# Optimization experiments

Hardware: AMD Instinct MI355X
Metric: run time of the kernel (lower is better)

Reference implementation:

```python
import jax, jax.numpy as jnp
import numpy as np

B, N, D_IN, D_OUT, H = 2, 2048, 1024, 1024, 16
HEAD_DIM = D_OUT // H


def setup_inputs() -> dict:
    key = jax.random.key(0)
    ks = jax.random.split(key, 8)
    s = 0.02
    return {
        "x": jax.random.normal(ks[0], (B, N, D_IN), dtype=jnp.float32),
        "Wq": jax.random.normal(ks[1], (D_IN, D_OUT), dtype=jnp.float32) * s,
        "Wk": jax.random.normal(ks[2], (D_IN, D_OUT), dtype=jnp.float32) * s,
        "Wv": jax.random.normal(ks[3], (D_IN, D_OUT), dtype=jnp.float32) * s,
        "Wo": jax.random.normal(ks[4], (D_OUT, D_OUT), dtype=jnp.float32) * s,
        "bo": jnp.zeros((D_OUT,), dtype=jnp.float32),
        "w": jax.random.uniform(ks[5], (H,), dtype=jnp.float32),
        "v": jax.random.uniform(ks[6], (H,), dtype=jnp.float32),
    }


def reference(x, Wq, Wk, Wv, Wo, bo, w, v):
    b, n, _ = x.shape
    h = w.shape[0]
    hd = Wq.shape[1] // h

    # QKV projections -> [b, h, n, hd]
    def proj(W):
        return (x @ W).reshape(b, n, h, hd).transpose(0, 2, 1, 3)

    q, k, val = proj(Wq), proj(Wk), proj(Wv)

    # relative-distance decay R_hat: [h, n, n]
    pos = jnp.arange(n)
    R = jnp.abs(pos[:, None] - pos[None, :]).astype(x.dtype)  # [n, n]
    wv = w[:, None, None]
    vv = v[:, None, None]
    R_hat = (1.0 + jnp.exp(vv)) / (1.0 + jnp.exp(vv - wv * R))  # [h, n, n]

    # ReLU(QK^T) * R_hat, causal mask, scaled softmax
    scores = jax.nn.relu(jnp.einsum("bhqd,bhkd->bhqk", q, k)) * R_hat[None]
    causal = jnp.triu(jnp.ones((n, n), dtype=bool), k=1)
    scores = jnp.where(causal[None, None], -jnp.inf, scores)
    attn = jax.nn.softmax(scores / np.sqrt(hd).astype(x.dtype), axis=-1)

    ctx = jnp.einsum("bhqk,bhkd->bhqd", attn, val)
    ctx = ctx.transpose(0, 2, 1, 3).reshape(b, n, h * hd)
    return ctx @ Wo + bo
```

## Files before the change

kernel.cpp:

```cpp
#include <hip/hip_runtime.h>

typedef unsigned short u16;
typedef unsigned int u32;
typedef __attribute__((ext_vector_type(8))) short bf16x8;
typedef __attribute__((ext_vector_type(4))) float f32x4;

__device__ __forceinline__ u16 f2bf(float f) {
    u32 u = __float_as_uint(f);
    u += 0x7fffu + ((u >> 16) & 1u);
    return (u16)(u >> 16);
}

#define GL2LDS(gp, lp)                                                                 \
    __builtin_amdgcn_global_load_lds((const __attribute__((address_space(1))) u32*)(const void*)(gp), \
                                     (__attribute__((address_space(3))) u32*)(void*)(lp), 16, 0, 0)

__global__ __launch_bounds__(256) void cast_kernel(const float* __restrict__ src,
                                                   u16* __restrict__ dst, int n4) {
    int i = blockIdx.x * 256 + threadIdx.x;
    if (i >= n4) return;
    float4 val = ((const float4*)src)[i];
    uint2 o;
    o.x = ((u32)f2bf(val.y) << 16) | f2bf(val.x);
    o.y = ((u32)f2bf(val.w) << 16) | f2bf(val.z);
    ((uint2*)dst)[i] = o;
}

__global__ __launch_bounds__(256) void transpose4(const float* __restrict__ Wq,
                                                  const float* __restrict__ Wk,
                                                  const float* __restrict__ Wv,
                                                  const float* __restrict__ Wo,
                                                  u16* __restrict__ Wcat,
                                                  u16* __restrict__ Wot) {
    __shared__ float tl[32][33];
    const int zi = blockIdx.z;
    const float* src = (zi == 0) ? Wq : (zi == 1) ? Wk : (zi == 2) ? Wv : Wo;
    u16* dst = (zi < 3) ? (Wcat + zi * 1048576) : Wot;
    const int tx = threadIdx.x & 31, ty = threadIdx.x >> 5;
    const int kt = blockIdx.y * 32, nt = blockIdx.x * 32;
#pragma unroll
    for (int j = 0; j < 4; ++j)
        tl[ty + j * 8][tx] = src[(kt + ty + j * 8) * 1024 + nt + tx];
    __syncthreads();
#pragma unroll
    for (int j = 0; j < 4; ++j)
        dst[(nt + ty + j * 8) * 1024 + kt + tx] = f2bf(tl[tx][ty + j * 8]);
}

__global__ __launch_bounds__(256) void rtab_kernel(const float* __restrict__ wp,
                                                   const float* __restrict__ vp,
                                                   float* __restrict__ tab,
                                                   u32* __restrict__ counter) {
    const int i = blockIdx.x * 256 + threadIdx.x;
    if (i == 0) counter[0] = 0u;
    const int h = i >> 11, d = i & 2047;
    const float vv = vp[h], ww = wp[h];
    tab[i] = (1.f + expf(vv)) / (1.f + expf(vv - ww * (float)d)) * 0.125f;
}

template <int MODE, int BN>
__global__ __launch_bounds__(256, 3) void gemm128(const u16* __restrict__ A,
                                                  const u16* __restrict__ Bt,
                                                  float* __restrict__ C,
                                                  const float* __restrict__ bias,
                                                  u16* __restrict__ Cb,
                                                  u16* __restrict__ Vtb,
                                                  int M, int N, int K) {
    constexpr int NBW = BN / 32;
    __shared__ __align__(16) u16 As[8192];
    __shared__ __align__(16) u16 Bs[BN * 64];
    const int t = threadIdx.x, lane = t & 63, wv = t >> 6;
    const int l15 = lane & 15, quad = lane >> 4;
    const int m0 = blockIdx.y << 7, n0 = blockIdx.x * BN;
    const int wm = (wv & 1) << 6, wn = (wv >> 1) * (BN / 2);

    f32x4 acc[4][NBW];
#pragma unroll
    for (int i = 0; i < 4; ++i)
#pragma unroll
        for (int j = 0; j < NBW; ++j) acc[i][j] = (f32x4){0.f, 0.f, 0.f, 0.f};

    const int lrow = lane >> 3, lchunk = lane & 7;
    for (int k0 = 0; k0 < K; k0 += 64) {
#pragma unroll
        for (int c = 0; c < 4; ++c) {
            const int r0 = wv * 32 + c * 8;
            const int row = r0 + lrow;
            const int g = lchunk ^ (row & 7);
            GL2LDS(A + (size_t)(m0 + row) * K + k0 + g * 8, &As[r0 * 64]);
        }
#pragma unroll
        for (int c = 0; c < BN / 32; ++c) {
            const int r0 = wv * (BN / 4) + c * 8;
            const int row = r0 + lrow;
            const int g = lchunk ^ (row & 7);
            GL2LDS(Bt + (size_t)(n0 + row) * K + k0 + g * 8, &Bs[r0 * 64]);
        }
        __syncthreads();
#pragma unroll
        for (int ks = 0; ks < 2; ++ks) {
            const int p = ((ks << 2) | quad) ^ (l15 & 7);
            bf16x8 af[4], bfr[NBW];
#pragma unroll
            for (int i = 0; i < 4; ++i)
                af[i] = *(const bf16x8*)&As[(wm + i * 16 + l15) * 64 + p * 8];
#pragma unroll
            for (int j = 0; j < NBW; ++j)
                bfr[j] = *(const bf16x8*)&Bs[(wn + j * 16 + l15) * 64 + p * 8];
#pragma unroll
            for (int mb = 0; mb < 4; ++mb)
#pragma unroll
                for (int nb = 0; nb < NBW; ++nb)
                    acc[mb][nb] = __builtin_amdgcn_mfma_f32_16x16x32_bf16(af[mb], bfr[nb],
                                                                          acc[mb][nb], 0, 0, 0);
        }
        __syncthreads();
    }
    const int rb = m0 + wm + (quad << 2);
    const int cbase = n0 + wn + l15;
#pragma unroll
    for (int mb = 0; mb < 4; ++mb)
#pragma unroll
        for (int nb = 0; nb < NBW; ++nb) {
            const int col = cbase + nb * 16;
#pragma unroll
            for (int r = 0; r < 4; ++r) {
                const int row = rb + mb * 16 + r;
                if (MODE == 0) {
                    C[(size_t)row * N + col] = acc[mb][nb][r] + bias[col];
                } else {
                    if (col < 2048)
                        Cb[(size_t)row * 2048 + col] = f2bf(acc[mb][nb][r]);
                    else
                        Vtb[(size_t)(col - 2048) * 4096 + row] = f2bf(acc[mb][nb][r]);
                }
            }
        }
}

__global__ __launch_bounds__(256, 3) void attn_kernel(const u16* __restrict__ qkb,
                                                      const u16* __restrict__ vtb,
                                                      const float* __restrict__ rtab,
                                                      u16* __restrict__ ctxb,
                                                      u32* __restrict__ counter) {
    __shared__ __align__(16) u16 Kt[2][4096];
    __shared__ __align__(16) u16 Vt2[2][4096];
    __shared__ __align__(16) u16 Ps[64][76];
    __shared__ float rall[2048];
    __shared__ float lred[4][64];
    __shared__ int jobS;

    const int t = threadIdx.x, lane = t & 63, wv = t >> 6;
    const int l15 = lane & 15, quad = lane >> 4;
    const int lrow = lane >> 3, lchunk = lane & 7;
    const int half0 = (wv & 1) * 32;

    for (;;) {
        if (t == 0) jobS = (int)atomicAdd(counter, 1u);
        __syncthreads();
        const int job = jobS;
        if (job >= 1024) break;
        const int qt = 31 - (job >> 5);
        const int bh = job & 31;
        const int b = bh >> 4, h = bh & 15;
        const int q0 = qt << 6;

        for (int i = t; i < q0 + 64; i += 256) rall[i] = rtab[(h << 11) + i];

        bf16x8 qa[4][2];
#pragma unroll
        for (int mb = 0; mb < 4; ++mb) {
            const u16* qrow = qkb + (size_t)(b * 2048 + q0 + mb * 16 + l15) * 2048 +
                              (h << 6) + quad * 8;
            qa[mb][0] = *(const bf16x8*)(qrow);
            qa[mb][1] = *(const bf16x8*)(qrow + 32);
        }

        f32x4 cacc[4];
#pragma unroll
        for (int i = 0; i < 4; ++i) cacc[i] = (f32x4){0.f, 0.f, 0.f, 0.f};
        float lacc[4][4] = {};

#pragma unroll
        for (int c = 0; c < 4; ++c) {
            const int r0 = half0 + c * 8;
            const int row = r0 + lrow;
            const int g = lchunk ^ (row & 7);
            if (wv < 2)
                GL2LDS(qkb + (size_t)(b * 2048 + row) * 2048 + 1024 + (h << 6) + g * 8,
                       &Kt[0][r0 * 64]);
            else
                GL2LDS(vtb + (size_t)((h << 6) + row) * 4096 + b * 2048 + g * 8,
                       &Vt2[0][r0 * 64]);
        }

        for (int kt = 0; kt <= qt; ++kt) {
            const int bsel = kt & 1;
            __syncthreads();
            if (kt < qt) {
                const int kg0 = (kt + 1) << 6;
#pragma unroll
                for (int c = 0; c < 4; ++c) {
                    const int r0 = half0 + c * 8;
                    const int row = r0 + lrow;
                    const int g = lchunk ^ (row & 7);
                    if (wv < 2)
                        GL2LDS(qkb + (size_t)(b * 2048 + kg0 + row) * 2048 + 1024 + (h << 6) + g * 8,
                               &Kt[bsel ^ 1][r0 * 64]);
                    else
                        GL2LDS(vtb + (size_t)((h << 6) + row) * 4096 + b * 2048 + kg0 + g * 8,
                               &Vt2[bsel ^ 1][r0 * 64]);
                }
            }

            f32x4 sacc[4];
#pragma unroll
            for (int i = 0; i < 4; ++i) sacc[i] = (f32x4){0.f, 0.f, 0.f, 0.f};
#pragma unroll
            for (int ks = 0; ks < 2; ++ks) {
                const int p = ((ks << 2) | quad) ^ (l15 & 7);
                bf16x8 kb = *(const bf16x8*)&Kt[bsel][((wv << 4) + l15) * 64 + p * 8];
#pragma unroll
                for (int mb = 0; mb < 4; ++mb)
                    sacc[mb] = __builtin_amdgcn_mfma_f32_16x16x32_bf16(qa[mb][ks], kb,
                                                                       sacc[mb], 0, 0, 0);
            }

            const int dbase = q0 - ((kt << 6) + (wv << 4) + l15);
            if (kt < qt) {
#pragma unroll
                for (int mb = 0; mb < 4; ++mb)
#pragma unroll
                    for (int r = 0; r < 4; ++r) {
                        const int dist = dbase + mb * 16 + (quad << 2) + r;
                        const float pe = __expf(fmaxf(sacc[mb][r], 0.f) * rall[dist]);
                        lacc[mb][r] += pe;
                        Ps[mb * 16 + (quad << 2) + r][(wv << 4) + l15] =
                            (u16)(__float_as_uint(pe) >> 16);
                    }
            } else {
#pragma unroll
                for (int mb = 0; mb < 4; ++mb)
#pragma unroll
                    for (int r = 0; r < 4; ++r) {
                        const int dist = dbase + mb * 16 + (quad << 2) + r;
                        const int di = dist < 0 ? 0 : dist;
                        float pe = __expf(fmaxf(sacc[mb][r], 0.f) * rall[di]);
                        pe = (dist < 0) ? 0.f : pe;
                        lacc[mb][r] += pe;
                        Ps[mb * 16 + (quad << 2) + r][(wv << 4) + l15] =
                            (u16)(__float_as_uint(pe) >> 16);
                    }
            }
            __syncthreads();

#pragma unroll
            for (int ks = 0; ks < 2; ++ks) {
                const int p = ((ks << 2) | quad) ^ (l15 & 7);
                bf16x8 vb = *(const bf16x8*)&Vt2[bsel][((wv << 4) + l15) * 64 + p * 8];
#pragma unroll
                for (int mb = 0; mb < 4; ++mb) {
                    bf16x8 pa = *(const bf16x8*)&Ps[mb * 16 + l15][ks * 32 + quad * 8];
                    cacc[mb] = __builtin_amdgcn_mfma_f32_16x16x32_bf16(pa, vb,
                                                                       cacc[mb], 0, 0, 0);
                }
            }
        }

#pragma unroll
        for (int off = 1; off < 16; off <<= 1)
#pragma unroll
            for (int mb = 0; mb < 4; ++mb)
#pragma unroll
                for (int r = 0; r < 4; ++r)
                    lacc[mb][r] += __shfl_xor(lacc[mb][r], off, 16);
        if (l15 == 0) {
#pragma unroll
            for (int mb = 0; mb < 4; ++mb)
#pragma unroll
                for (int r = 0; r < 4; ++r)
                    lred[wv][mb * 16 + (quad << 2) + r] = lacc[mb][r];
        }
        __syncthreads();
#pragma unroll
        for (int mb = 0; mb < 4; ++mb)
#pragma unroll
            for (int r = 0; r < 4; ++r) {
                const int row = mb * 16 + (quad << 2) + r;
                const float lt = (lred[0][row] + lred[1][row]) + (lred[2][row] + lred[3][row]);
                const float o = cacc[mb][r] / lt;
                ctxb[(size_t)(b * 2048 + q0 + row) * 1024 + (h << 6) + (wv << 4) + l15] = f2bf(o);
            }
    }
}

extern "C" void kernel_launch(void* const* d_in, const int* in_sizes, int n_in,
                              void* d_out, int out_size, void* d_ws, size_t ws_size,
                              hipStream_t stream) {
    const float* x  = (const float*)d_in[0];
    const float* Wq = (const float*)d_in[1];
    const float* Wk = (const float*)d_in[2];
    const float* Wv = (const float*)d_in[3];
    const float* Wo = (const float*)d_in[4];
    const float* bo = (const float*)d_in[5];
    const float* w  = (const float*)d_in[6];
    const float* v  = (const float*)d_in[7];
    float* out = (float*)d_out;

    char* w8 = (char*)d_ws;
    u16*  xb   = (u16*)(w8);
    u16*  Wcat = (u16*)(w8 + (8u << 20));
    u16*  Wot  = (u16*)(w8 + (14u << 20));
    u16*  qkb  = (u16*)(w8 + (16u << 20));
    u16*  vtb  = (u16*)(w8 + (32u << 20));
    u16*  ctxb = (u16*)(w8 + (40u << 20));
    float* rtab = (float*)(w8 + (48u << 20));
    u32*  counter = (u32*)(w8 + (48u << 20) + (1u << 17));

    cast_kernel<<<4096, 256, 0, stream>>>(x, xb, 1048576);
    transpose4<<<dim3(32, 32, 4), 256, 0, stream>>>(Wq, Wk, Wv, Wo, Wcat, Wot);
    rtab_kernel<<<128, 256, 0, stream>>>(w, v, rtab, counter);

    gemm128<1, 128><<<dim3(24, 32), 256, 0, stream>>>(xb, Wcat, nullptr, nullptr, qkb, vtb,
                                                      4096, 3072, 1024);
    attn_kernel<<<768, 256, 0, stream>>>(qkb, vtb, rtab, ctxb, counter);
    gemm128<0, 64><<<dim3(16, 32), 256, 0, stream>>>(ctxb, Wot, out, bo, nullptr, nullptr,
                                                     4096, 1024, 1024);
}
```

Before: 196.6 us.

## Keep attention probabilities in registers via transposed MFMA; add separate V transpose

The attention kernel now computes S^T (K as the A operand, Q as B), so each wave owns 16 query rows. The exp'd probabilities are packed straight into bf16 MFMA operands in registers, which removes the Ps shared-memory round trip, a barrier per key tile, and the cross-wave row-sum reduction through LDS. V is read from LDS with split 8-byte loads to match the new operand layout. The QKV GEMM now writes V row-major with coalesced stores, and a new tiled transpose kernel produces the transposed V, replacing the scattered strided stores at the cost of one extra launch and an extra pass over V.

Measured after the change: 193.3 us. No clear change (-1.7%).

```diff
diff --git a/kernel.cpp b/kernel.cpp
--- a/kernel.cpp
+++ b/kernel.cpp
@@ -47,6 +47,31 @@
         dst[(nt + ty + j * 8) * 1024 + kt + tx] = f2bf(tl[tx][ty + j * 8]);
 }
 
+__global__ __launch_bounds__(256) void transpose_v(const u16* __restrict__ src,
+                                                   u16* __restrict__ dst) {
+    __shared__ u16 tl[64][68];
+    const int t = threadIdx.x, tx = t & 15, ty = t >> 4;
+    const int rt = blockIdx.y * 64, ct = blockIdx.x * 64;
+#pragma unroll
+    for (int j = 0; j < 4; ++j) {
+        const int row = ty + j * 16;
+        uint2 vv = *(const uint2*)(src + (size_t)(rt + row) * 1024 + ct + tx * 4);
+        tl[row][tx * 4 + 0] = (u16)(vv.x & 0xffff);
+        tl[row][tx * 4 + 1] = (u16)(vv.x >> 16);
+        tl[row][tx * 4 + 2] = (u16)(vv.y & 0xffff);
+        tl[row][tx * 4 + 3] = (u16)(vv.y >> 16);
+    }
+    __syncthreads();
+#pragma unroll
+    for (int j = 0; j < 4; ++j) {
+        const int c = ty + j * 16;
+        uint2 o;
+        o.x = (u32)tl[tx * 4 + 0][c] | ((u32)tl[tx * 4 + 1][c] << 16);
+        o.y = (u32)tl[tx * 4 + 2][c] | ((u32)tl[tx * 4 + 3][c] << 16);
+        *(uint2*)(dst + (size_t)(ct + c) * 4096 + rt + tx * 4) = o;
+    }
+}
+
 __global__ __launch_bounds__(256) void rtab_kernel(const float* __restrict__ wp,
                                                    const float* __restrict__ vp,
                                                    float* __restrict__ tab,
@@ -64,7 +89,7 @@
                                                   float* __restrict__ C,
                                                   const float* __restrict__ bias,
                                                   u16* __restrict__ Cb,
-                                                  u16* __restrict__ Vtb,
+                                                  u16* __restrict__ Vrow,
                                                   int M, int N, int K) {
     constexpr int NBW = BN / 32;
     __shared__ __align__(16) u16 As[8192];
@@ -132,7 +157,7 @@
                     if (col < 2048)
                         Cb[(size_t)row * 2048 + col] = f2bf(acc[mb][nb][r]);
                     else
-                        Vtb[(size_t)(col - 2048) * 4096 + row] = f2bf(acc[mb][nb][r]);
+                        Vrow[(size_t)row * 1024 + (col - 2048)] = f2bf(acc[mb][nb][r]);
                 }
             }
         }
@@ -145,9 +170,7 @@
                                                       u32* __restrict__ counter) {
     __shared__ __align__(16) u16 Kt[2][4096];
     __shared__ __align__(16) u16 Vt2[2][4096];
-    __shared__ __align__(16) u16 Ps[64][76];
     __shared__ float rall[2048];
-    __shared__ float lred[4][64];
     __shared__ int jobS;
 
     const int t = threadIdx.x, lane = t & 63, wv = t >> 6;
@@ -167,19 +190,18 @@
 
         for (int i = t; i < q0 + 64; i += 256) rall[i] = rtab[(h << 11) + i];
 
-        bf16x8 qa[4][2];
-#pragma unroll
-        for (int mb = 0; mb < 4; ++mb) {
-            const u16* qrow = qkb + (size_t)(b * 2048 + q0 + mb * 16 + l15) * 2048 +
+        bf16x8 qb[2];
+        {
+            const u16* qrow = qkb + (size_t)(b * 2048 + q0 + (wv << 4) + l15) * 2048 +
                               (h << 6) + quad * 8;
-            qa[mb][0] = *(const bf16x8*)(qrow);
-            qa[mb][1] = *(const bf16x8*)(qrow + 32);
+            qb[0] = *(const bf16x8*)(qrow);
+            qb[1] = *(const bf16x8*)(qrow + 32);
         }
 
         f32x4 cacc[4];
 #pragma unroll
         for (int i = 0; i < 4; ++i) cacc[i] = (f32x4){0.f, 0.f, 0.f, 0.f};
-        float lacc[4][4] = {};
+        float lacc = 0.f;
 
 #pragma unroll
         for (int c = 0; c < 4; ++c) {
@@ -219,78 +241,84 @@
 #pragma unroll
             for (int ks = 0; ks < 2; ++ks) {
                 const int p = ((ks << 2) | quad) ^ (l15 & 7);
-                bf16x8 kb = *(const bf16x8*)&Kt[bsel][((wv << 4) + l15) * 64 + p * 8];
-#pragma unroll
-                for (int mb = 0; mb < 4; ++mb)
-                    sacc[mb] = __builtin_amdgcn_mfma_f32_16x16x32_bf16(qa[mb][ks], kb,
+#pragma unroll
+                for (int mb = 0; mb < 4; ++mb) {
+                    bf16x8 ka = *(const bf16x8*)&Kt[bsel][(mb * 16 + l15) * 64 + p * 8];
+                    sacc[mb] = __builtin_amdgcn_mfma_f32_16x16x32_bf16(ka, qb[ks],
                                                                        sacc[mb], 0, 0, 0);
-            }
-
-            const int dbase = q0 - ((kt << 6) + (wv << 4) + l15);
+                }
+            }
+
+            const int D0 = q0 - (kt << 6) + (wv << 4) + l15;
+            u32 pk[4][2];
             if (kt < qt) {
 #pragma unroll
-                for (int mb = 0; mb < 4; ++mb)
+                for (int mb = 0; mb < 4; ++mb) {
+                    float pe[4];
 #pragma unroll
                     for (int r = 0; r < 4; ++r) {
-                        const int dist = dbase + mb * 16 + (quad << 2) + r;
-                        const float pe = __expf(fmaxf(sacc[mb][r], 0.f) * rall[dist]);
-                        lacc[mb][r] += pe;
-                        Ps[mb * 16 + (quad << 2) + r][(wv << 4) + l15] =
-                            (u16)(__float_as_uint(pe) >> 16);
+                        const int dist = D0 - (mb * 16 + (quad << 2) + r);
+                        pe[r] = __expf(fmaxf(sacc[mb][r], 0.f) * rall[dist]);
+                        lacc += pe[r];
                     }
+                    pk[mb][0] = (__float_as_uint(pe[0]) >> 16) |
+                                (__float_as_uint(pe[1]) & 0xffff0000u);
+                    pk[mb][1] = (__float_as_uint(pe[2]) >> 16) |
+                                (__float_as_uint(pe[3]) & 0xffff0000u);
+                }
             } else {
 #pragma unroll
-                for (int mb = 0; mb < 4; ++mb)
+                for (int mb = 0; mb < 4; ++mb) {
+                    float pe[4];
 #pragma unroll
                     for (int r = 0; r < 4; ++r) {
-                        const int dist = dbase + mb * 16 + (quad << 2) + r;
+                        const int dist = D0 - (mb * 16 + (quad << 2) + r);
                         const int di = dist < 0 ? 0 : dist;
-                        float pe = __expf(fmaxf(sacc[mb][r], 0.f) * rall[di]);
-                        pe = (dist < 0) ? 0.f : pe;
-                        lacc[mb][r] += pe;
-                        Ps[mb * 16 + (quad << 2) + r][(wv << 4) + l15] =
-                            (u16)(__float_as_uint(pe) >> 16);
+                        float p0 = __expf(fmaxf(sacc[mb][r], 0.f) * rall[di]);
+                        pe[r] = (dist < 0) ? 0.f : p0;
+                        lacc += pe[r];
                     }
-            }
-            __syncthreads();
+                    pk[mb][0] = (__float_as_uint(pe[0]) >> 16) |
+                                (__float_as_uint(pe[1]) & 0xffff0000u);
+                    pk[mb][1] = (__float_as_uint(pe[2]) >> 16) |
+                                (__float_as_uint(pe[3]) & 0xffff0000u);
+                }
+            }
 
 #pragma unroll
             for (int ks = 0; ks < 2; ++ks) {
-                const int p = ((ks << 2) | quad) ^ (l15 & 7);
-                bf16x8 vb = *(const bf16x8*)&Vt2[bsel][((wv << 4) + l15) * 64 + p * 8];
-#pragma unroll
-                for (int mb = 0; mb < 4; ++mb) {
-                    bf16x8 pa = *(const bf16x8*)&Ps[mb * 16 + l15][ks * 32 + quad * 8];
-                    cacc[mb] = __builtin_amdgcn_mfma_f32_16x16x32_bf16(pa, vb,
-                                                                       cacc[mb], 0, 0, 0);
-                }
-            }
-        }
-
-#pragma unroll
-        for (int off = 1; off < 16; off <<= 1)
-#pragma unroll
-            for (int mb = 0; mb < 4; ++mb)
-#pragma unroll
-                for (int r = 0; r < 4; ++r)
-                    lacc[mb][r] += __shfl_xor(lacc[mb][r], off, 16);
-        if (l15 == 0) {
-#pragma unroll
-            for (int mb = 0; mb < 4; ++mb)
-#pragma unroll
-                for (int r = 0; r < 4; ++r)
-                    lred[wv][mb * 16 + (quad << 2) + r] = lacc[mb][r];
-        }
-        __syncthreads();
-#pragma unroll
-        for (int mb = 0; mb < 4; ++mb)
-#pragma unroll
-            for (int r = 0; r < 4; ++r) {
-                const int row = mb * 16 + (quad << 2) + r;
-                const float lt = (lred[0][row] + lred[1][row]) + (lred[2][row] + lred[3][row]);
-                const float o = cacc[mb][r] / lt;
-                ctxb[(size_t)(b * 2048 + q0 + row) * 1024 + (h << 6) + (wv << 4) + l15] = f2bf(o);
-            }
+                int4 pv = {(int)pk[2 * ks][0], (int)pk[2 * ks][1],
+                           (int)pk[2 * ks + 1][0], (int)pk[2 * ks + 1][1]};
+                bf16x8 pb = *(bf16x8*)&pv;
+                const int gA = (4 * ks + (quad >> 1)) ^ (l15 & 7);
+                const int gB = (4 * ks + 2 + (quad >> 1)) ^ (l15 & 7);
+                const int off = (quad & 1) * 4;
+#pragma unroll
+                for (int db = 0; db < 4; ++db) {
+                    const u16* base = &Vt2[bsel][(db * 16 + l15) * 64];
+                    uint2 va = *(const uint2*)(base + gA * 8 + off);
+                    uint2 vb = *(const uint2*)(base + gB * 8 + off);
+                    int4 vv = {(int)va.x, (int)va.y, (int)vb.x, (int)vb.y};
+                    bf16x8 vf = *(bf16x8*)&vv;
+                    cacc[db] = __builtin_amdgcn_mfma_f32_16x16x32_bf16(vf, pb,
+                                                                       cacc[db], 0, 0, 0);
+                }
+            }
+        }
+
+        float lt = lacc;
+        lt += __shfl_xor(lt, 16, 64);
+        lt += __shfl_xor(lt, 32, 64);
+        const float inv = 1.f / lt;
+        u16* op = ctxb + (size_t)(b * 2048 + q0 + (wv << 4) + l15) * 1024 +
+                  (h << 6) + (quad << 2);
+#pragma unroll
+        for (int db = 0; db < 4; ++db) {
+            uint2 o;
+            o.x = (u32)f2bf(cacc[db][0] * inv) | ((u32)f2bf(cacc[db][1] * inv) << 16);
+            o.y = (u32)f2bf(cacc[db][2] * inv) | ((u32)f2bf(cacc[db][3] * inv) << 16);
+            *(uint2*)(op + db * 16) = o;
+        }
     }
 }
 
@@ -316,13 +344,15 @@
     u16*  ctxb = (u16*)(w8 + (40u << 20));
     float* rtab = (float*)(w8 + (48u << 20));
     u32*  counter = (u32*)(w8 + (48u << 20) + (1u << 17));
+    u16*  vrow = (u16*)(w8 + (49u << 20));
 
     cast_kernel<<<4096, 256, 0, stream>>>(x, xb, 1048576);
     transpose4<<<dim3(32, 32, 4), 256, 0, stream>>>(Wq, Wk, Wv, Wo, Wcat, Wot);
     rtab_kernel<<<128, 256, 0, stream>>>(w, v, rtab, counter);
 
-    gemm128<1, 128><<<dim3(24, 32), 256, 0, stream>>>(xb, Wcat, nullptr, nullptr, qkb, vtb,
+    gemm128<1, 128><<<dim3(24, 32), 256, 0, stream>>>(xb, Wcat, nullptr, nullptr, qkb, vrow,
                                                       4096, 3072, 1024);
+    transpose_v<<<dim3(16, 64), 256, 0, stream>>>(vrow, vtb);
     attn_kernel<<<768, 256, 0, stream>>>(qkb, vtb, rtab, ctxb, counter);
     gemm128<0, 64><<<dim3(16, 32), 256, 0, stream>>>(ctxb, Wot, out, bo, nullptr, nullptr,
                                                      4096, 1024, 1024);
```
